# Performance work log

Hardware: AMD Instinct MI355X
Metric: run time of the kernel (lower is better)

The kernel has to match this reference:

```python
import jax, jax.numpy as jnp
import numpy as np
from functools import partial

EPS = 1e-5


def _positions(size, step, ps):
    """Static top/left offsets of overlapping windows, mimicking patch_divide loops."""
    pos = []
    for i in range(0, size + step - ps, step):
        t = i
        if i + ps > size:
            t = size - ps
        pos.append(t)
    return np.asarray(pos, dtype=np.int32)


def _div_factor(size, step, ps):
    """Multiplicative factor replicating the sequential /=2 strips in patch_reverse."""
    f = np.ones(size, dtype=np.float32)
    for i in range(step, size + step - ps, step):
        top, down = i, i + ps - step
        if top + ps > size:
            top = size - ps
        f[top:down] *= 0.5
    return f


def _layernorm(x, w, b):
    m = jnp.mean(x, axis=-1, keepdims=True)
    v = jnp.var(x, axis=-1, keepdims=True)
    return (x - m) / jnp.sqrt(v + EPS) * w + b


def _gelu(x):
    return jax.nn.gelu(x, approximate=False)


def setup_inputs() -> dict:
    key = jax.random.key(0)
    ks = jax.random.split(key, 8)
    dim, qk_dim, mlp_dim = 96, 64, 192
    b, h, w = 2, 256, 256
    s = lambda fan: 1.0 / np.sqrt(fan)
    return {
        "x": jax.random.normal(ks[0], (b, dim, h, w), jnp.float32),
        "norm1_w": jnp.ones((dim,), jnp.float32),
        "norm1_b": jnp.zeros((dim,), jnp.float32),
        "wq": jax.random.normal(ks[1], (dim, qk_dim), jnp.float32) * s(dim),
        "wk": jax.random.normal(ks[2], (dim, qk_dim), jnp.float32) * s(dim),
        "wv": jax.random.normal(ks[3], (dim, dim), jnp.float32) * s(dim),
        "wproj": jax.random.normal(ks[4], (dim, dim), jnp.float32) * s(dim),
        "norm2_w": jnp.ones((dim,), jnp.float32),
        "norm2_b": jnp.zeros((dim,), jnp.float32),
        "fc1_w": jax.random.normal(ks[5], (dim, mlp_dim), jnp.float32) * s(dim),
        "fc1_b": jnp.zeros((mlp_dim,), jnp.float32),
        "dw_w": jax.random.normal(ks[6], (mlp_dim, 1, 5, 5), jnp.float32) * s(25),
        "dw_b": jnp.zeros((mlp_dim,), jnp.float32),
        "fc2_w": jax.random.normal(ks[7], (mlp_dim, dim), jnp.float32) * s(mlp_dim),
        "fc2_b": jnp.zeros((dim,), jnp.float32),
        "ps": 16,
    }


HEADS = 4


def reference(x, norm1_w, norm1_b, wq, wk, wv, wproj, norm2_w, norm2_b,
              fc1_w, fc1_b, dw_w, dw_b, fc2_w, fc2_b, ps):
    b, c, h, w = x.shape
    step = ps - 2
    if h == ps and w == ps:
        step = ps

    tops = _positions(h, step, ps)
    lefts = _positions(w, step, ps)
    nh, nw = len(tops), len(lefts)
    n = nh * nw
    row_idx = tops[:, None] + np.arange(ps)    # (nh, ps)
    col_idx = lefts[:, None] + np.arange(ps)   # (nw, ps)

    # ---- patch_divide: gather overlapping windows -> (b*n, ps*ps, c) ----
    crop = x[:, :, row_idx[:, None, :, None], col_idx[None, :, None, :]]  # (b,c,nh,nw,ps,ps)
    tok = crop.transpose(0, 2, 3, 4, 5, 1).reshape(b * n, ps * ps, c)

    # ---- PreNorm + Attention (F.sdpa default scale = 1/sqrt(head_dim)) ----
    y = _layernorm(tok, norm1_w, norm1_b)
    qk_dim = wq.shape[1]
    hd_q = qk_dim // HEADS
    hd_v = c // HEADS
    q = (y @ wq).reshape(b * n, ps * ps, HEADS, hd_q).transpose(0, 2, 1, 3)
    k = (y @ wk).reshape(b * n, ps * ps, HEADS, hd_q).transpose(0, 2, 1, 3)
    v = (y @ wv).reshape(b * n, ps * ps, HEADS, hd_v).transpose(0, 2, 1, 3)
    scores = jnp.einsum('bhnd,bhmd->bhnm', q, k) / jnp.sqrt(jnp.float32(hd_q))
    attn = jax.nn.softmax(scores, axis=-1)
    out = jnp.einsum('bhnm,bhmd->bhnd', attn, v)
    out = out.transpose(0, 2, 1, 3).reshape(b * n, ps * ps, c)
    tok = out @ wproj + tok  # residual

    # ---- patch_reverse: overlap-add scatter + strip averaging ----
    crop = tok.reshape(b, nh, nw, ps, ps, c).transpose(0, 5, 1, 2, 3, 4)  # (b,c,nh,nw,ps,ps)
    acc = jnp.zeros_like(x)
    acc = acc.at[:, :, row_idx[:, None, :, None], col_idx[None, :, None, :]].add(crop)
    fh = jnp.asarray(_div_factor(h, step, ps))
    fw = jnp.asarray(_div_factor(w, step, ps))
    x2 = acc * fh[None, None, :, None] * fw[None, None, None, :]

    # ---- PreNorm + ConvFFN on full image tokens ----
    tok2 = x2.transpose(0, 2, 3, 1).reshape(b, h * w, c)
    y = _layernorm(tok2, norm2_w, norm2_b)
    y = _gelu(y @ fc1_w + fc1_b)                       # (b, hw, mlp)
    mlp = y.shape[-1]
    ymap = y.transpose(0, 2, 1).reshape(b, mlp, h, w)  # NCHW
    dw = jax.lax.conv_general_dilated(
        ymap, dw_w, window_strides=(1, 1), padding=((2, 2), (2, 2)),
        dimension_numbers=('NCHW', 'OIHW', 'NCHW'), feature_group_count=mlp)
    dw = _gelu(dw + dw_b[None, :, None, None])
    y = y + dw.reshape(b, mlp, h * w).transpose(0, 2, 1)
    tok2 = (y @ fc2_w + fc2_b) + tok2  # residual

    return tok2.reshape(b, h, w, c).transpose(0, 3, 1, 2)
```

## Files before the change

### kernel.cpp

```cpp
#include <hip/hip_runtime.h>

typedef unsigned short u16;
typedef unsigned int u32;
typedef __attribute__((ext_vector_type(8))) short bf16x8;
typedef __attribute__((ext_vector_type(4))) float f32x4;

__device__ __forceinline__ float US2F(u16 u) {
    return __uint_as_float(((u32)u) << 16);
}
__device__ __forceinline__ u16 F2US(float f) {
    u32 u = __float_as_uint(f);
    u32 rounding = 0x7fffu + ((u >> 16) & 1u);
    u += rounding;
    return (u16)(u >> 16);
}

__device__ __forceinline__ int win_pos(int i) { return (i == 18) ? 240 : 14 * i; }
__device__ __forceinline__ float gelu_exact(float x) {
    return 0.5f * x * (1.0f + erff(x * 0.7071067811865475f));
}

__global__ __launch_bounds__(256) void k_prep(
    const float* __restrict__ wq, const float* __restrict__ wk, const float* __restrict__ wv,
    const float* __restrict__ wproj, const float* __restrict__ fc1w, const float* __restrict__ fc2w,
    u16* __restrict__ wT)
{
    int i = blockIdx.x * 256 + threadIdx.x;
    if (i < 21504) {
        int m = i / 96, c = i % 96;
        float v = (m < 64) ? wq[c * 64 + m] : ((m < 128) ? wk[c * 64 + m - 64] : wv[c * 96 + m - 128]);
        wT[i] = F2US(v);
    } else if (i < 30720) {
        int j = i - 21504; int n = j / 96, k = j % 96;
        wT[i] = F2US(wproj[k * 96 + n]);
    } else if (i < 49152) {
        int j = i - 30720; int n = j / 96, k = j % 96;
        wT[i] = F2US(fc1w[k * 192 + n]);
    } else if (i < 67584) {
        int j = i - 49152; int n = j / 192, k = j % 192;
        wT[i] = F2US(fc2w[k * 96 + n]);
    }
}

#define YSTR 104
__global__ __launch_bounds__(256) void k_ln_qkv_mfma(
    const float* __restrict__ x, const float* __restrict__ n1w, const float* __restrict__ n1b,
    const u16* __restrict__ wqkvT, u16* __restrict__ qkv)
{
    __shared__ __align__(16) u16 ys[256 * YSTR];
    int wi = blockIdx.x;
    int b = wi / 361, r = wi % 361;
    int top = win_pos(r / 19), lf = win_pos(r % 19);
    int t = threadIdx.x;
    int gy = top + (t >> 4), gx = lf + (t & 15);
    const float* xp = x + (long)b * 96 * 65536 + (long)gy * 256 + gx;

    float s = 0.f, ss = 0.f;
    for (int c = 0; c < 96; ++c) {
        float v = xp[(long)c * 65536];
        ys[t * YSTR + c] = F2US(v);
        s += v; ss += v * v;
    }
    float mu = s * (1.f / 96.f);
    float var = ss * (1.f / 96.f) - mu * mu;
    float rstd = rsqrtf(var + 1e-5f);
    for (int c = 0; c < 96; ++c) {
        float v = US2F(ys[t * YSTR + c]);
        ys[t * YSTR + c] = F2US((v - mu) * rstd * n1w[c] + n1b[c]);
    }
    __syncthreads();

    int wvid = t >> 6, lane = t & 63, l15 = lane & 15, kg = lane >> 4;
    const f32x4 zc = {0.f, 0.f, 0.f, 0.f};

    for (int i = 0; i < 4; ++i) {
        int rt = wvid * 4 + i;
        bf16x8 a0 = *(const bf16x8*)(ys + (rt * 16 + l15) * YSTR + 0  + kg * 8);
        bf16x8 a1 = *(const bf16x8*)(ys + (rt * 16 + l15) * YSTR + 32 + kg * 8);
        bf16x8 a2 = *(const bf16x8*)(ys + (rt * 16 + l15) * YSTR + 64 + kg * 8);
        for (int nt = 0; nt < 14; ++nt) {
            const u16* wp = wqkvT + (nt * 16 + l15) * 96 + kg * 8;
            f32x4 acc = __builtin_amdgcn_mfma_f32_16x16x32_bf16(a0, *(const bf16x8*)(wp), zc, 0, 0, 0);
            acc = __builtin_amdgcn_mfma_f32_16x16x32_bf16(a1, *(const bf16x8*)(wp + 32), acc, 0, 0, 0);
            acc = __builtin_amdgcn_mfma_f32_16x16x32_bf16(a2, *(const bf16x8*)(wp + 64), acc, 0, 0, 0);
            u16* op = qkv + ((long)wi * 256 + rt * 16 + kg * 4) * 224 + nt * 16 + l15;
            #pragma unroll
            for (int rr = 0; rr < 4; ++rr) op[rr * 224] = F2US(acc[rr]);
        }
    }
}

#define PSTR 264
__global__ __launch_bounds__(128) void k_attn_mfma(const u16* __restrict__ qkv, u16* __restrict__ attn)
{
    __shared__ __align__(16) u16 vt[2][24 * PSTR];
    __shared__ __align__(16) u16 pls[2][16 * PSTR];

    int wi = blockIdx.x >> 1;
    int pairid = blockIdx.x & 1;
    int wvv = threadIdx.x >> 6;
    int hd = pairid * 2 + wvv;
    int lane = threadIdx.x & 63;
    int l15 = lane & 15;
    int kg = lane >> 4;

    const u16* base = qkv + (long)wi * 256 * 224;
    u16* vtp = vt[wvv];
    u16* plp = pls[wvv];

    const bf16x8 zf = {0,0,0,0,0,0,0,0};
    const f32x4 zc = {0.f,0.f,0.f,0.f};

    for (int rd = 0; rd < 4; ++rd) {
        int tok = rd * 64 + lane;
        const u16* vp = base + tok * 224 + 128 + hd * 24;
        bf16x8 v0 = *(const bf16x8*)(vp);
        bf16x8 v1 = *(const bf16x8*)(vp + 8);
        bf16x8 v2 = *(const bf16x8*)(vp + 16);
        #pragma unroll
        for (int j = 0; j < 8; ++j) {
            vtp[(j)      * PSTR + tok] = (u16)v0[j];
            vtp[(j + 8)  * PSTR + tok] = (u16)v1[j];
            vtp[(j + 16) * PSTR + tok] = (u16)v2[j];
        }
    }

    bf16x8 kfr[16];
    #pragma unroll
    for (int nt = 0; nt < 16; ++nt) {
        int key = nt * 16 + l15;
        kfr[nt] = (kg < 2) ? *(const bf16x8*)(base + key * 224 + 64 + hd * 16 + kg * 8) : zf;
    }
    __syncthreads();

    for (int qt = 0; qt < 16; ++qt) {
        int qtok = qt * 16 + l15;
        bf16x8 qfr = (kg < 2) ? *(const bf16x8*)(base + qtok * 224 + hd * 16 + kg * 8) : zf;

        f32x4 S[16];
        #pragma unroll
        for (int nt = 0; nt < 16; ++nt)
            S[nt] = __builtin_amdgcn_mfma_f32_16x16x32_bf16(qfr, kfr[nt], zc, 0, 0, 0);

        #pragma unroll
        for (int nt = 0; nt < 16; ++nt) S[nt] *= 0.25f;

        float mx[4];
        #pragma unroll
        for (int r = 0; r < 4; ++r) {
            float m = S[0][r];
            #pragma unroll
            for (int nt = 1; nt < 16; ++nt) m = fmaxf(m, S[nt][r]);
            #pragma unroll
            for (int msk = 1; msk < 16; msk <<= 1) m = fmaxf(m, __shfl_xor(m, msk));
            mx[r] = m;
        }
        #pragma unroll
        for (int nt = 0; nt < 16; ++nt) {
            #pragma unroll
            for (int r = 0; r < 4; ++r) S[nt][r] = __expf(S[nt][r] - mx[r]);
        }
        float li[4];
        #pragma unroll
        for (int r = 0; r < 4; ++r) {
            float s = S[0][r];
            #pragma unroll
            for (int nt = 1; nt < 16; ++nt) s += S[nt][r];
            #pragma unroll
            for (int msk = 1; msk < 16; msk <<= 1) s += __shfl_xor(s, msk);
            li[r] = 1.f / s;
        }
        #pragma unroll
        for (int nt = 0; nt < 16; ++nt) {
            #pragma unroll
            for (int r = 0; r < 4; ++r) {
                int R = kg * 4 + r;
                plp[R * PSTR + nt * 16 + l15] = F2US(S[nt][r]);
            }
        }
        __syncthreads();

        f32x4 O0 = zc, O1 = zc;
        int vd1 = 16 + l15;
        #pragma unroll
        for (int ks = 0; ks < 8; ++ks) {
            bf16x8 af = *(const bf16x8*)(plp + l15 * PSTR + ks * 32 + kg * 8);
            bf16x8 b0 = *(const bf16x8*)(vtp + l15 * PSTR + ks * 32 + kg * 8);
            bf16x8 b1 = (l15 < 8) ? *(const bf16x8*)(vtp + vd1 * PSTR + ks * 32 + kg * 8) : zf;
            O0 = __builtin_amdgcn_mfma_f32_16x16x32_bf16(af, b0, O0, 0, 0, 0);
            O1 = __builtin_amdgcn_mfma_f32_16x16x32_bf16(af, b1, O1, 0, 0, 0);
        }
        #pragma unroll
        for (int r = 0; r < 4; ++r) {
            int R = kg * 4 + r;
            long tok = (long)wi * 256 + qt * 16 + R;
            attn[tok * 96 + hd * 24 + l15] = F2US(O0[r] * li[r]);
            if (l15 < 8) attn[tok * 96 + hd * 24 + 16 + l15] = F2US(O1[r] * li[r]);
        }
        __syncthreads();
    }
}

#define WOSTR 264
__global__ __launch_bounds__(256) void k_proj_mfma(
    const u16* __restrict__ attn, const u16* __restrict__ wprojT,
    u16* __restrict__ wout)
{
    __shared__ __align__(16) u16 cs[96 * WOSTR];
    int wi = blockIdx.x;
    int t = threadIdx.x;
    int wvid = t >> 6, lane = t & 63, l15 = lane & 15, kg = lane >> 4;
    const f32x4 zc = {0.f, 0.f, 0.f, 0.f};

    for (int i = 0; i < 4; ++i) {
        int rt = wvid * 4 + i;
        const u16* ap = attn + ((long)wi * 256 + rt * 16 + l15) * 96 + kg * 8;
        bf16x8 a0 = *(const bf16x8*)(ap);
        bf16x8 a1 = *(const bf16x8*)(ap + 32);
        bf16x8 a2 = *(const bf16x8*)(ap + 64);
        for (int nt = 0; nt < 6; ++nt) {
            const u16* wp = wprojT + (nt * 16 + l15) * 96 + kg * 8;
            f32x4 acc = __builtin_amdgcn_mfma_f32_16x16x32_bf16(a0, *(const bf16x8*)(wp), zc, 0, 0, 0);
            acc = __builtin_amdgcn_mfma_f32_16x16x32_bf16(a1, *(const bf16x8*)(wp + 32), acc, 0, 0, 0);
            acc = __builtin_amdgcn_mfma_f32_16x16x32_bf16(a2, *(const bf16x8*)(wp + 64), acc, 0, 0, 0);
            int c = nt * 16 + l15;
            #pragma unroll
            for (int rr = 0; rr < 4; ++rr) {
                int tok = rt * 16 + kg * 4 + rr;
                cs[c * WOSTR + tok] = F2US(acc[rr]);
            }
        }
    }
    __syncthreads();
    u16* wo = wout + (long)wi * 24576;
    for (int seg = t; seg < 3072; seg += 256) {
        int c = seg >> 5, t8 = (seg & 31) << 3;
        *(bf16x8*)(wo + c * 256 + t8) = *(const bf16x8*)(cs + c * WOSTR + t8);
    }
}

__global__ __launch_bounds__(256) void k_gather(
    const u16* __restrict__ wout, const float* __restrict__ x, float* __restrict__ accb)
{
    int blk = blockIdx.x;
    int y = blk & 255;
    int c = (blk >> 8) % 96;
    int b = blk / (96 * 256);
    int xx = threadIdx.x;

    int iyl[2]; int ny = 0;
    {
        int c1 = min(17, y / 14), c0 = c1 - 1;
        if (c0 >= 0 && y >= 14 * c0 && y < 14 * c0 + 16) iyl[ny++] = c0;
        if (y >= 14 * c1 && y < 14 * c1 + 16) iyl[ny++] = c1;
        if (y >= 240) iyl[ny++] = 18;
    }
    int ixl[2]; int nx = 0;
    {
        int c1 = min(17, xx / 14), c0 = c1 - 1;
        if (c0 >= 0 && xx >= 14 * c0 && xx < 14 * c0 + 16) ixl[nx++] = c0;
        if (xx >= 14 * c1 && xx < 14 * c1 + 16) ixl[nx++] = c1;
        if (xx >= 240) ixl[nx++] = 18;
    }

    long p = (long)(b * 96 + c) * 65536 + y * 256 + xx;
    float v = (float)(ny * nx) * x[p];
    for (int a = 0; a < ny; ++a) {
        int ty = win_pos(iyl[a]);
        int rowoff = (y - ty) * 16;
        for (int e = 0; e < nx; ++e) {
            int tx = win_pos(ixl[e]);
            int wi = b * 361 + iyl[a] * 19 + ixl[e];
            v += US2F(wout[(long)wi * 24576 + c * 256 + rowoff + (xx - tx)]);
        }
    }
    float f = ((ny == 2) ? 0.5f : 1.f) * ((nx == 2) ? 0.5f : 1.f);
    accb[p] = v * f;
}

#define XASTR 104
__global__ __launch_bounds__(256) void k_ln2_fc1_mfma(
    const float* __restrict__ accb,
    const float* __restrict__ n2w, const float* __restrict__ n2b,
    const u16* __restrict__ fc1T, const float* __restrict__ fc1b,
    u16* __restrict__ y1)
{
    __shared__ float xs[64 * 97];
    __shared__ __align__(16) u16 xa[64 * XASTR];
    __shared__ float mu_s[64], rs_s[64];
    int p0 = blockIdx.x * 64;
    int b = p0 >> 16, pp = p0 & 65535;
    int tid = threadIdx.x;

    for (int idx = tid; idx < 64 * 96; idx += 256) {
        int c = idx >> 6, px = idx & 63;
        xs[px * 97 + c] = accb[(long)(b * 96 + c) * 65536 + pp + px];
    }
    __syncthreads();
    if (tid < 64) {
        float s = 0.f, ss = 0.f;
        for (int c = 0; c < 96; ++c) { float v = xs[tid * 97 + c]; s += v; ss += v * v; }
        float mu = s * (1.f / 96.f);
        float var = ss * (1.f / 96.f) - mu * mu;
        mu_s[tid] = mu; rs_s[tid] = rsqrtf(var + 1e-5f);
    }
    __syncthreads();
    for (int idx = tid; idx < 64 * 96; idx += 256) {
        int c = idx >> 6, px = idx & 63;
        xa[px * XASTR + c] = F2US((xs[px * 97 + c] - mu_s[px]) * rs_s[px] * n2w[c] + n2b[c]);
    }
    __syncthreads();

    int wvid = tid >> 6, lane = tid & 63, l15 = lane & 15, kg = lane >> 4;
    const f32x4 zc = {0.f, 0.f, 0.f, 0.f};
    bf16x8 a0 = *(const bf16x8*)(xa + (wvid * 16 + l15) * XASTR + 0  + kg * 8);
    bf16x8 a1 = *(const bf16x8*)(xa + (wvid * 16 + l15) * XASTR + 32 + kg * 8);
    bf16x8 a2 = *(const bf16x8*)(xa + (wvid * 16 + l15) * XASTR + 64 + kg * 8);

    for (int nt = 0; nt < 12; ++nt) {
        const u16* wp = fc1T + (nt * 16 + l15) * 96 + kg * 8;
        f32x4 acc = __builtin_amdgcn_mfma_f32_16x16x32_bf16(a0, *(const bf16x8*)(wp), zc, 0, 0, 0);
        acc = __builtin_amdgcn_mfma_f32_16x16x32_bf16(a1, *(const bf16x8*)(wp + 32), acc, 0, 0, 0);
        acc = __builtin_amdgcn_mfma_f32_16x16x32_bf16(a2, *(const bf16x8*)(wp + 64), acc, 0, 0, 0);
        int m = nt * 16 + l15;
        float bb = fc1b[m];
        ushort4 pk;
        pk.x = F2US(gelu_exact(acc[0] + bb));
        pk.y = F2US(gelu_exact(acc[1] + bb));
        pk.z = F2US(gelu_exact(acc[2] + bb));
        pk.w = F2US(gelu_exact(acc[3] + bb));
        *(ushort4*)(y1 + (long)(b * 192 + m) * 65536 + pp + wvid * 16 + kg * 4) = pk;
    }
}

__global__ __launch_bounds__(256) void k_dwconv(
    const u16* __restrict__ y1, const float* __restrict__ dww, const float* __restrict__ dwb,
    u16* __restrict__ y2)
{
    __shared__ float tile[20 * 68];
    int blk = blockIdx.x;
    int txt = blk & 3;
    int tyt = (blk >> 2) & 15;
    int m   = (blk >> 6) % 192;
    int b   = blk / (64 * 192);
    int bx = txt * 64, by = tyt * 16;
    int tid = threadIdx.x;

    const u16* plane = y1 + (long)(b * 192 + m) * 65536;
    for (int idx = tid; idx < 20 * 68; idx += 256) {
        int ly = idx / 68, lx = idx - ly * 68;
        int sy = by + ly - 2, sx = bx + lx - 2;
        float v = 0.f;
        if (sy >= 0 && sy < 256 && sx >= 0 && sx < 256) v = US2F(plane[sy * 256 + sx]);
        tile[idx] = v;
    }
    float w[25];
    #pragma unroll
    for (int j = 0; j < 25; ++j) w[j] = dww[m * 25 + j];
    float bias = dwb[m];
    __syncthreads();

    int tx = tid & 63, ty0 = tid >> 6;
    u16* oplane = y2 + (long)(b * 192 + m) * 65536;
    #pragma unroll
    for (int i = 0; i < 4; ++i) {
        int ty = ty0 * 4 + i;
        float acc = 0.f;
        #pragma unroll
        for (int ky = 0; ky < 5; ++ky)
            #pragma unroll
            for (int kx = 0; kx < 5; ++kx)
                acc += tile[(ty + ky) * 68 + tx + kx] * w[ky * 5 + kx];
        float center = tile[(ty + 2) * 68 + tx + 2];
        float v = center + gelu_exact(acc + bias);
        oplane[(by + ty) * 256 + bx + tx] = F2US(v);
    }
}

#define Y2STR 200
__global__ __launch_bounds__(256) void k_fc2_mfma(
    const u16* __restrict__ y2, const u16* __restrict__ fc2T, const float* __restrict__ fc2b,
    const float* __restrict__ accb, float* __restrict__ out)
{
    __shared__ __align__(16) u16 ys2[64 * Y2STR];
    int p0 = blockIdx.x * 64;
    int b = p0 >> 16, pp = p0 & 65535;
    int tid = threadIdx.x;
    for (int idx = tid; idx < 64 * 192; idx += 256) {
        int m = idx >> 6, px = idx & 63;
        ys2[px * Y2STR + m] = y2[(long)(b * 192 + m) * 65536 + pp + px];
    }
    __syncthreads();

    int wvid = tid >> 6, lane = tid & 63, l15 = lane & 15, kg = lane >> 4;
    const f32x4 zc = {0.f, 0.f, 0.f, 0.f};
    bf16x8 af[6];
    #pragma unroll
    for (int ks = 0; ks < 6; ++ks)
        af[ks] = *(const bf16x8*)(ys2 + (wvid * 16 + l15) * Y2STR + ks * 32 + kg * 8);

    int pxb = pp + wvid * 16 + kg * 4;

    for (int nt = 0; nt < 6; ++nt) {
        const u16* wp = fc2T + (nt * 16 + l15) * 192 + kg * 8;
        f32x4 acc = zc;
        #pragma unroll
        for (int ks = 0; ks < 6; ++ks)
            acc = __builtin_amdgcn_mfma_f32_16x16x32_bf16(af[ks], *(const bf16x8*)(wp + ks * 32), acc, 0, 0, 0);
        int c = nt * 16 + l15;
        long gbase = (long)(b * 96 + c) * 65536 + pxb;
        float4 av = *(const float4*)(accb + gbase);
        float4 res;
        float bb = fc2b[c];
        res.x = acc[0] + bb + av.x;
        res.y = acc[1] + bb + av.y;
        res.z = acc[2] + bb + av.z;
        res.w = acc[3] + bb + av.w;
        *(float4*)(out + gbase) = res;
    }
}

extern "C" void kernel_launch(void* const* d_in, const int* in_sizes, int n_in,
                              void* d_out, int out_size, void* d_ws, size_t ws_size,
                              hipStream_t stream)
{
    const float* x     = (const float*)d_in[0];
    const float* n1w   = (const float*)d_in[1];
    const float* n1b   = (const float*)d_in[2];
    const float* wq    = (const float*)d_in[3];
    const float* wk    = (const float*)d_in[4];
    const float* wv    = (const float*)d_in[5];
    const float* wproj = (const float*)d_in[6];
    const float* n2w   = (const float*)d_in[7];
    const float* n2b   = (const float*)d_in[8];
    const float* fc1w  = (const float*)d_in[9];
    const float* fc1b  = (const float*)d_in[10];
    const float* dww   = (const float*)d_in[11];
    const float* dwb   = (const float*)d_in[12];
    const float* fc2w  = (const float*)d_in[13];
    const float* fc2b  = (const float*)d_in[14];

    char* ws = (char*)d_ws;
    float* accb = (float*)ws;
    u16* qkv  = (u16*)(ws + 50331648);
    u16* attn = (u16*)(ws + 133136384);
    u16* wout = (u16*)(ws + 50331648);
    u16* y1   = (u16*)(ws + 100663296);
    u16* y2   = (u16*)(ws + 50331648);
    u16* wT   = (u16*)(ws + 168624128);
    u16* wqkvT  = wT;
    u16* wprojT = wT + 21504;
    u16* fc1T   = wT + 30720;
    u16* fc2T   = wT + 49152;
    float* out = (float*)d_out;

    k_prep<<<264, 256, 0, stream>>>(wq, wk, wv, wproj, fc1w, fc2w, wT);
    k_ln_qkv_mfma<<<722, 256, 0, stream>>>(x, n1w, n1b, wqkvT, qkv);
    k_attn_mfma<<<1444, 128, 0, stream>>>(qkv, attn);
    k_proj_mfma<<<722, 256, 0, stream>>>(attn, wprojT, wout);
    k_gather<<<49152, 256, 0, stream>>>(wout, x, accb);
    k_ln2_fc1_mfma<<<2048, 256, 0, stream>>>(accb, n2w, n2b, fc1T, fc1b, y1);
    k_dwconv<<<24576, 256, 0, stream>>>(y1, dww, dwb, y2);
    k_fc2_mfma<<<2048, 256, 0, stream>>>(y2, fc2T, fc2b, accb, out);
}
```

Before: 529.2 us.

## Keep softmax probabilities in registers via transposed QK^T and lane shuffles

The attention kernel now computes the transposed score tile by swapping the MFMA operands, so each lane holds four keys for a single query. Softmax runs without max subtraction, and the sum is reduced with two cross-lane shuffles. Probabilities are packed to bf16 with v_cvt_pk_bf16 and rearranged into the PV MFMA A-operand layout with xor shuffles, which removes the shared-memory round trip and the block barriers. A launch-bounds occupancy hint is added. Dropping the max subtraction risks overflow if the scaled scores are large.

```diff
diff --git a/kernel.cpp b/kernel.cpp
--- a/kernel.cpp
+++ b/kernel.cpp
@@ -4,6 +4,7 @@
 typedef unsigned int u32;
 typedef __attribute__((ext_vector_type(8))) short bf16x8;
 typedef __attribute__((ext_vector_type(4))) float f32x4;
+typedef __attribute__((ext_vector_type(4))) u32 u32x4;
 
 __device__ __forceinline__ float US2F(u16 u) {
     return __uint_as_float(((u32)u) << 16);
@@ -13,6 +14,11 @@
     u32 rounding = 0x7fffu + ((u >> 16) & 1u);
     u += rounding;
     return (u16)(u >> 16);
+}
+__device__ __forceinline__ u32 cvt_pk_bf16(float lo, float hi) {
+    u32 d;
+    asm("v_cvt_pk_bf16_f32 %0, %1, %2" : "=v"(d) : "v"(lo), "v"(hi));
+    return d;
 }
 
 __device__ __forceinline__ int win_pos(int i) { return (i == 18) ? 240 : 14 * i; }
@@ -91,10 +97,9 @@
 }
 
 #define PSTR 264
-__global__ __launch_bounds__(128) void k_attn_mfma(const u16* __restrict__ qkv, u16* __restrict__ attn)
+__global__ __launch_bounds__(128, 3) void k_attn_mfma(const u16* __restrict__ qkv, u16* __restrict__ attn)
 {
     __shared__ __align__(16) u16 vt[2][24 * PSTR];
-    __shared__ __align__(16) u16 pls[2][16 * PSTR];
 
     int wi = blockIdx.x >> 1;
     int pairid = blockIdx.x & 1;
@@ -103,10 +108,10 @@
     int lane = threadIdx.x & 63;
     int l15 = lane & 15;
     int kg = lane >> 4;
+    int b4 = kg & 1, b5 = kg >> 1;
 
     const u16* base = qkv + (long)wi * 256 * 224;
     u16* vtp = vt[wvv];
-    u16* plp = pls[wvv];
 
     const bf16x8 zf = {0,0,0,0,0,0,0,0};
     const f32x4 zc = {0.f,0.f,0.f,0.f};
@@ -131,73 +136,67 @@
         int key = nt * 16 + l15;
         kfr[nt] = (kg < 2) ? *(const bf16x8*)(base + key * 224 + 64 + hd * 16 + kg * 8) : zf;
     }
-    __syncthreads();
 
     for (int qt = 0; qt < 16; ++qt) {
         int qtok = qt * 16 + l15;
         bf16x8 qfr = (kg < 2) ? *(const bf16x8*)(base + qtok * 224 + hd * 16 + kg * 8) : zf;
 
-        f32x4 S[16];
-        #pragma unroll
-        for (int nt = 0; nt < 16; ++nt)
-            S[nt] = __builtin_amdgcn_mfma_f32_16x16x32_bf16(qfr, kfr[nt], zc, 0, 0, 0);
-
-        #pragma unroll
-        for (int nt = 0; nt < 16; ++nt) S[nt] *= 0.25f;
-
-        float mx[4];
-        #pragma unroll
-        for (int r = 0; r < 4; ++r) {
-            float m = S[0][r];
-            #pragma unroll
-            for (int nt = 1; nt < 16; ++nt) m = fmaxf(m, S[nt][r]);
-            #pragma unroll
-            for (int msk = 1; msk < 16; msk <<= 1) m = fmaxf(m, __shfl_xor(m, msk));
-            mx[r] = m;
-        }
+        u32 pk[16][2];
+        float ssum = 0.f;
         #pragma unroll
         for (int nt = 0; nt < 16; ++nt) {
-            #pragma unroll
-            for (int r = 0; r < 4; ++r) S[nt][r] = __expf(S[nt][r] - mx[r]);
-        }
-        float li[4];
-        #pragma unroll
-        for (int r = 0; r < 4; ++r) {
-            float s = S[0][r];
-            #pragma unroll
-            for (int nt = 1; nt < 16; ++nt) s += S[nt][r];
-            #pragma unroll
-            for (int msk = 1; msk < 16; msk <<= 1) s += __shfl_xor(s, msk);
-            li[r] = 1.f / s;
-        }
-        #pragma unroll
-        for (int nt = 0; nt < 16; ++nt) {
-            #pragma unroll
-            for (int r = 0; r < 4; ++r) {
-                int R = kg * 4 + r;
-                plp[R * PSTR + nt * 16 + l15] = F2US(S[nt][r]);
-            }
-        }
-        __syncthreads();
+            f32x4 S = __builtin_amdgcn_mfma_f32_16x16x32_bf16(kfr[nt], qfr, zc, 0, 0, 0);
+            float p0 = __expf(S[0] * 0.25f);
+            float p1 = __expf(S[1] * 0.25f);
+            float p2 = __expf(S[2] * 0.25f);
+            float p3 = __expf(S[3] * 0.25f);
+            ssum += (p0 + p1) + (p2 + p3);
+            pk[nt][0] = cvt_pk_bf16(p0, p1);
+            pk[nt][1] = cvt_pk_bf16(p2, p3);
+        }
+        ssum += __shfl_xor(ssum, 16);
+        ssum += __shfl_xor(ssum, 32);
+        float li = 1.f / ssum;
 
         f32x4 O0 = zc, O1 = zc;
         int vd1 = 16 + l15;
         #pragma unroll
         for (int ks = 0; ks < 8; ++ks) {
-            bf16x8 af = *(const bf16x8*)(plp + l15 * PSTR + ks * 32 + kg * 8);
+            u32 A0 = pk[2*ks][0],   A1 = pk[2*ks][1];
+            u32 B0 = pk[2*ks+1][0], B1 = pk[2*ks+1][1];
+            u32 x0 = b4 ? A0 : B0;
+            u32 x1 = b4 ? A1 : B1;
+            u32 r0 = __shfl_xor((int)x0, 16);
+            u32 r1 = __shfl_xor((int)x1, 16);
+            u32 c0 = b4 ? r0 : A0;
+            u32 c1 = b4 ? r1 : A1;
+            u32 c2 = b4 ? B0 : r0;
+            u32 c3 = b4 ? B1 : r1;
+            u32 g0 = __shfl_xor((int)c0, 48);
+            u32 g1 = __shfl_xor((int)c1, 48);
+            u32 g2 = __shfl_xor((int)c2, 48);
+            u32 g3 = __shfl_xor((int)c3, 48);
+            bool diag = (b4 == b5);
+            u32x4 fv;
+            fv.x = diag ? c0 : g0;
+            fv.y = diag ? c1 : g1;
+            fv.z = diag ? c2 : g2;
+            fv.w = diag ? c3 : g3;
+            bf16x8 pa = __builtin_bit_cast(bf16x8, fv);
+
             bf16x8 b0 = *(const bf16x8*)(vtp + l15 * PSTR + ks * 32 + kg * 8);
             bf16x8 b1 = (l15 < 8) ? *(const bf16x8*)(vtp + vd1 * PSTR + ks * 32 + kg * 8) : zf;
-            O0 = __builtin_amdgcn_mfma_f32_16x16x32_bf16(af, b0, O0, 0, 0, 0);
-            O1 = __builtin_amdgcn_mfma_f32_16x16x32_bf16(af, b1, O1, 0, 0, 0);
+            O0 = __builtin_amdgcn_mfma_f32_16x16x32_bf16(pa, b0, O0, 0, 0, 0);
+            O1 = __builtin_amdgcn_mfma_f32_16x16x32_bf16(pa, b1, O1, 0, 0, 0);
         }
         #pragma unroll
         for (int r = 0; r < 4; ++r) {
+            float lq = __shfl(li, kg * 4 + r);
             int R = kg * 4 + r;
             long tok = (long)wi * 256 + qt * 16 + R;
-            attn[tok * 96 + hd * 24 + l15] = F2US(O0[r] * li[r]);
-            if (l15 < 8) attn[tok * 96 + hd * 24 + 16 + l15] = F2US(O1[r] * li[r]);
-        }
-        __syncthreads();
+            attn[tok * 96 + hd * 24 + l15] = F2US(O0[r] * lq);
+            if (l15 < 8) attn[tok * 96 + hd * 24 + 16 + l15] = F2US(O1[r] * lq);
+        }
     }
 }
 
```

New measurement: 474.5 us. 10.3% less time.
